# Optimization experiments

Measured on AMD Instinct MI355X. Metric: run time of the kernel, lower is better.

Reference implementation:

```python
import jax, jax.numpy as jnp
import numpy as np

B, T, C, NH = 8, 1024, 1024, 16
DH = C // NH  # 64


def setup_inputs() -> dict:
    key = jax.random.key(0)
    ks = jax.random.split(key, 7)
    s = 1.0 / np.sqrt(C)
    return {
        "x": jax.random.normal(ks[0], (B, T, C), dtype=jnp.float32),
        "Wq": jax.random.normal(ks[1], (C, C), dtype=jnp.float32) * s,
        "bq": jnp.zeros((C,), dtype=jnp.float32),
        "Wk": jax.random.normal(ks[2], (C, C), dtype=jnp.float32) * s,
        "bk": jnp.zeros((C,), dtype=jnp.float32),
        "Wv": jax.random.normal(ks[3], (C, C), dtype=jnp.float32) * s,
        "bv": jnp.zeros((C,), dtype=jnp.float32),
    }


def reference(x, Wq, bq, Wk, bk, Wv, bv):
    # Linear projections (weights stored as [in, out])
    q = x @ Wq + bq  # [B, T, C]
    k = x @ Wk + bk
    v = x @ Wv + bv
    q = q.reshape(B, T, NH, DH)
    k = k.reshape(B, T, NH, DH)
    v = v.reshape(B, T, NH, DH)
    scale = 1.0 / np.sqrt(DH)
    # NOTE: source module's causal mask buffer is all-ones due to a non-inplace
    # masked_fill bug, so attention is NON-causal (mask multiply is a no-op).
    attn = jnp.einsum("bqhd,bkhd->bhqk", q, k) * scale  # [B, NH, T, T]
    attn = jax.nn.softmax(attn, axis=-1)
    # dropout is identity (p=0 / eval)
    o = jnp.einsum("bhqk,bkhd->bqhd", attn, v)  # [B, T, NH, DH]
    return o.reshape(B, T, C)
```

## Files before the change

### kernel.cpp

```cpp
#include <hip/hip_runtime.h>


#define B_  8
#define T_  1024
#define C_  1024
#define NH_ 16
#define DH_ 64
#define M_  (B_ * T_)

typedef __bf16 bf16x8 __attribute__((ext_vector_type(8)));
typedef float  floatx4 __attribute__((ext_vector_type(4)));
typedef float  floatx16 __attribute__((ext_vector_type(16)));
typedef unsigned int uintx4 __attribute__((ext_vector_type(4)));

__device__ __forceinline__ unsigned short f2bf(float f) {
    unsigned int u = __float_as_uint(f);
    unsigned int r = (u + 0x7fffu + ((u >> 16) & 1u)) >> 16;
    return (unsigned short)r;
}

__device__ __forceinline__ unsigned int f2bf2(float a, float b) {
    unsigned int ua = __float_as_uint(a), ub = __float_as_uint(b);
    ua += 0x7fffu + ((ua >> 16) & 1u);
    ub += 0x7fffu + ((ub >> 16) & 1u);
#if __has_builtin(__builtin_amdgcn_perm)
    return __builtin_amdgcn_perm(ub, ua, 0x07060302u);
#else
    return (ua >> 16) | (ub & 0xffff0000u);
#endif
}

__device__ __forceinline__ void gload_lds16(const void* g, void* l) {
    __builtin_amdgcn_global_load_lds(
        (const __attribute__((address_space(1))) unsigned int*)g,
        (__attribute__((address_space(3))) unsigned int*)l, 16, 0, 0);
}

__global__ __launch_bounds__(256) void prep_kernel(
    const float* __restrict__ x, unsigned short* __restrict__ xb,
    const float* __restrict__ Wq, const float* __restrict__ Wk,
    const float* __restrict__ Wv, unsigned short* __restrict__ WtAll)
{
    int blk = blockIdx.x;
    if (blk < 8192) {
        int i = blk * 256 + threadIdx.x;
        float4 v = ((const float4*)x)[i];
        ushort4 o;
        unsigned int lo = f2bf2(v.x, v.y), hi = f2bf2(v.z, v.w);
        o.x = (unsigned short)lo; o.y = (unsigned short)(lo >> 16);
        o.z = (unsigned short)hi; o.w = (unsigned short)(hi >> 16);
        ((ushort4*)xb)[i] = o;
        return;
    }
    int tb3 = blk - 8192;
    int which = tb3 >> 8;
    int tb = tb3 & 255;
    const float* W = (which == 0) ? Wq : ((which == 1) ? Wk : Wv);
    unsigned short* out = WtAll + (size_t)which * C_ * C_;

    __shared__ __align__(16) unsigned short tile[64 * 68];
    int k0 = (tb >> 4) * 64, n0 = (tb & 15) * 64;
    int c = threadIdx.x & 63, r0 = threadIdx.x >> 6;

    for (int j = 0; j < 16; ++j) {
        int r = r0 + j * 4;
        tile[c * 68 + r] = f2bf(W[(size_t)(k0 + r) * C_ + n0 + c]);
    }
    __syncthreads();
    int k4 = (threadIdx.x & 15) * 4;
    int nw = threadIdx.x >> 4;
    for (int it = 0; it < 4; ++it) {
        int n = nw + it * 16;
        ushort4 o = *(const ushort4*)&tile[n * 68 + k4];
        *(ushort4*)&out[(size_t)(n0 + n) * C_ + k0 + k4] = o;
    }
}

__global__ __launch_bounds__(256) void qkv_gemm_kernel(
    const unsigned short* __restrict__ xb,
    const unsigned short* __restrict__ WtAll,
    const float* __restrict__ bq, const float* __restrict__ bk,
    const float* __restrict__ bv,
    unsigned short* __restrict__ Qb, unsigned short* __restrict__ Kb,
    unsigned short* __restrict__ Vt)
{
    int which = blockIdx.z;
    const unsigned short* W = WtAll + (size_t)which * C_ * C_;
    const float* bias = (which == 0) ? bq : ((which == 1) ? bk : bv);
    float oscale = (which == 0) ? 0.125f * 1.44269504f : 1.0f;

    __shared__ __align__(16) unsigned short As[128 * 64];
    __shared__ __align__(16) unsigned short Bs[128 * 64];

    int tid = threadIdx.x;
    int wave = tid >> 6, lane = tid & 63;
    int quad = lane >> 4, l16 = lane & 15, l7 = l16 & 7;
    int wm = wave >> 1, wn = wave & 1;
    int bm = blockIdx.x, bn = blockIdx.y;

    floatx4 acc[4][4] = {};

    for (int kk = 0; kk < C_; kk += 64) {
        __syncthreads();
        #pragma unroll
        for (int i = 0; i < 4; ++i) {
            int c = (wave * 4 + i) * 64 + lane;
            int row = c >> 3;
            int lcol = ((c & 7) ^ (row & 7)) * 8;
            gload_lds16(&xb[(size_t)(bm * 128 + row) * C_ + kk + lcol],
                        &As[(wave * 4 + i) * 512]);
            gload_lds16(&W[(size_t)(bn * 128 + row) * C_ + kk + lcol],
                        &Bs[(wave * 4 + i) * 512]);
        }
        __syncthreads();
        #pragma unroll
        for (int s = 0; s < 2; ++s) {
            bf16x8 a[4], bfr[4];
            #pragma unroll
            for (int mt = 0; mt < 4; ++mt) {
                int row = wm * 64 + mt * 16 + l16;
                a[mt] = *(const bf16x8*)&As[row * 64 + ((s * 4 + quad) ^ l7) * 8];
            }
            #pragma unroll
            for (int nt = 0; nt < 4; ++nt) {
                int row = wn * 64 + nt * 16 + l16;
                bfr[nt] = *(const bf16x8*)&Bs[row * 64 + ((s * 4 + quad) ^ l7) * 8];
            }
            if (which < 2) {
                #pragma unroll
                for (int mt = 0; mt < 4; ++mt)
                    #pragma unroll
                    for (int nt = 0; nt < 4; ++nt)
                        acc[mt][nt] = __builtin_amdgcn_mfma_f32_16x16x32_bf16(
                            bfr[nt], a[mt], acc[mt][nt], 0, 0, 0);
            } else {
                #pragma unroll
                for (int mt = 0; mt < 4; ++mt)
                    #pragma unroll
                    for (int nt = 0; nt < 4; ++nt)
                        acc[mt][nt] = __builtin_amdgcn_mfma_f32_16x16x32_bf16(
                            a[mt], bfr[nt], acc[mt][nt], 0, 0, 0);
            }
        }
    }

    if (which < 2) {
        unsigned short* outp = (which == 0) ? Qb : Kb;
        #pragma unroll
        for (int mt = 0; mt < 4; ++mt) {
            int tg = bm * 128 + wm * 64 + mt * 16 + l16;
            int bb = tg >> 10, t = tg & (T_ - 1);
            #pragma unroll
            for (int nt = 0; nt < 4; ++nt) {
                int colg = bn * 128 + wn * 64 + nt * 16 + quad * 4;
                int h = colg >> 6, d = colg & 63;
                float4 b4 = *(const float4*)&bias[colg];
                uint2 o;
                o.x = f2bf2((acc[mt][nt][0] + b4.x) * oscale,
                            (acc[mt][nt][1] + b4.y) * oscale);
                o.y = f2bf2((acc[mt][nt][2] + b4.z) * oscale,
                            (acc[mt][nt][3] + b4.w) * oscale);
                *(uint2*)&outp[((size_t)(bb * NH_ + h) * T_ + t) * DH_ + d] = o;
            }
        }
    } else {
        #pragma unroll
        for (int nt = 0; nt < 4; ++nt) {
            int colg = bn * 128 + wn * 64 + nt * 16 + l16;
            int h = colg >> 6, d = colg & 63;
            float bval = bias[colg];
            #pragma unroll
            for (int mt = 0; mt < 4; ++mt) {
                int tg = bm * 128 + wm * 64 + mt * 16 + quad * 4;
                int bb = tg >> 10, t = tg & (T_ - 1);
                uint2 o;
                o.x = f2bf2(acc[mt][nt][0] + bval, acc[mt][nt][1] + bval);
                o.y = f2bf2(acc[mt][nt][2] + bval, acc[mt][nt][3] + bval);
                *(uint2*)&Vt[((size_t)(bb * NH_ + h) * DH_ + d) * T_ + t] = o;
            }
        }
    }
}

__global__ __launch_bounds__(256) void attn_kernel(
    const unsigned short* __restrict__ Qb,
    const unsigned short* __restrict__ Kb,
    const unsigned short* __restrict__ Vt,
    float* __restrict__ out)
{
    int bh = blockIdx.x;
    int qblk = blockIdx.y;
    int b = bh >> 4, h = bh & (NH_ - 1);
    int tid = threadIdx.x;
    int wave = tid >> 6, lane = tid & 63;
    int l5 = lane & 31, hi = lane >> 5;

    const unsigned short* Qh = Qb + (size_t)bh * T_ * DH_;
    const unsigned short* Kh = Kb + (size_t)bh * T_ * DH_;
    const unsigned short* Vh = Vt + (size_t)bh * DH_ * T_;

    __shared__ __align__(16) unsigned short Ks[128 * 64];
    __shared__ __align__(16) unsigned short Vs[64 * 128];

    int qrow = qblk * 128 + wave * 32 + l5;
    bf16x8 qa[4];
    #pragma unroll
    for (int sl = 0; sl < 4; ++sl)
        qa[sl] = *(const bf16x8*)&Qh[(size_t)qrow * DH_ + sl * 16 + hi * 8];

    floatx16 o_acc[2] = {};
    float l_i = 0.0f;

    for (int kt2 = 0; kt2 < T_ / 128; ++kt2) {
        __syncthreads();
        #pragma unroll
        for (int i = 0; i < 4; ++i) {
            int c = (wave * 4 + i) * 64 + lane;
            int krow = c >> 3;
            int klcol = ((c & 7) ^ (krow & 7)) * 8;
            gload_lds16(&Kh[(size_t)(kt2 * 128 + krow) * DH_ + klcol],
                        &Ks[(wave * 4 + i) * 512]);
            int vrow = c >> 4;
            int vlcol = ((c & 15) ^ (vrow & 15)) * 8;
            gload_lds16(&Vh[(size_t)vrow * T_ + kt2 * 128 + vlcol],
                        &Vs[(wave * 4 + i) * 512]);
        }
        __syncthreads();

        #pragma unroll
        for (int kh = 0; kh < 2; ++kh) {
            #pragma unroll
            for (int nt = 0; nt < 2; ++nt) {
                floatx16 st = {};
                int r = kh * 64 + nt * 32 + l5;
                #pragma unroll
                for (int sl = 0; sl < 4; ++sl) {
                    bf16x8 kb = *(const bf16x8*)&Ks[r * 64 + ((sl * 2 + hi) ^ (r & 7)) * 8];
                    st = __builtin_amdgcn_mfma_f32_32x32x16_bf16(kb, qa[sl], st, 0, 0, 0);
                }

                unsigned int pd[8];
                float rs = 0.0f;
                #pragma unroll
                for (int m = 0; m < 8; ++m) {
                    float e0 = exp2f(st[2 * m]);
                    float e1 = exp2f(st[2 * m + 1]);
                    rs += e0 + e1;
                    pd[m] = f2bf2(e0, e1);
                }
                l_i += rs;

                #pragma unroll
                for (int ks2 = 0; ks2 < 2; ++ks2) {
                    int base = ks2 * 4;
                    uintx4 pbu;
                    {
                        unsigned int c0 = pd[base + 0], c2 = pd[base + 2];
                        unsigned int uk = hi ? c2 : c0;
                        unsigned int us = hi ? c0 : c2;
                        unsigned int rr = (unsigned int)__shfl_xor((int)us, 32);
                        pbu.x = hi ? rr : uk;
                        pbu.z = hi ? uk : rr;
                        unsigned int c1 = pd[base + 1], c3 = pd[base + 3];
                        uk = hi ? c3 : c1;
                        us = hi ? c1 : c3;
                        rr = (unsigned int)__shfl_xor((int)us, 32);
                        pbu.y = hi ? rr : uk;
                        pbu.w = hi ? uk : rr;
                    }
                    bf16x8 pb = __builtin_bit_cast(bf16x8, pbu);
                    int ch = (kh * 4 + nt * 2 + ks2) * 2 + hi;
                    #pragma unroll
                    for (int dt = 0; dt < 2; ++dt) {
                        int vr = dt * 32 + l5;
                        bf16x8 vb = *(const bf16x8*)&Vs[vr * 128 + (ch ^ (vr & 15)) * 8];
                        o_acc[dt] = __builtin_amdgcn_mfma_f32_32x32x16_bf16(
                            vb, pb, o_acc[dt], 0, 0, 0);
                    }
                }
            }
        }
    }

    float lt = l_i + __shfl_xor(l_i, 32);
    float inv = 1.0f / lt;
    int t = qblk * 128 + wave * 32 + l5;
    float* op = &out[((size_t)b * T_ + t) * C_ + h * DH_];
    #pragma unroll
    for (int dt = 0; dt < 2; ++dt) {
        #pragma unroll
        for (int g = 0; g < 4; ++g) {
            float4 v;
            v.x = o_acc[dt][g * 4 + 0] * inv;
            v.y = o_acc[dt][g * 4 + 1] * inv;
            v.z = o_acc[dt][g * 4 + 2] * inv;
            v.w = o_acc[dt][g * 4 + 3] * inv;
            *(float4*)&op[dt * 32 + g * 8 + hi * 4] = v;
        }
    }
}

extern "C" void kernel_launch(void* const* d_in, const int* in_sizes, int n_in,
                              void* d_out, int out_size, void* d_ws, size_t ws_size,
                              hipStream_t stream) {
    const float* x  = (const float*)d_in[0];
    const float* Wq = (const float*)d_in[1];
    const float* bq = (const float*)d_in[2];
    const float* Wk = (const float*)d_in[3];
    const float* bk = (const float*)d_in[4];
    const float* Wv = (const float*)d_in[5];
    const float* bv = (const float*)d_in[6];
    float* out = (float*)d_out;

    char* ws = (char*)d_ws;
    size_t off = 0;
    unsigned short* xb = (unsigned short*)(ws + off); off += (size_t)M_ * C_ * 2;
    unsigned short* Wt = (unsigned short*)(ws + off); off += (size_t)3 * C_ * C_ * 2;
    unsigned short* Qb = (unsigned short*)(ws + off); off += (size_t)M_ * C_ * 2;
    unsigned short* Kb = (unsigned short*)(ws + off); off += (size_t)M_ * C_ * 2;
    unsigned short* Vt = (unsigned short*)(ws + off); off += (size_t)M_ * C_ * 2;

    prep_kernel<<<dim3(8960), dim3(256), 0, stream>>>(x, xb, Wq, Wk, Wv, Wt);

    qkv_gemm_kernel<<<dim3(M_ / 128, C_ / 128, 3), dim3(256), 0, stream>>>(
        xb, Wt, bq, bk, bv, Qb, Kb, Vt);

    attn_kernel<<<dim3(B_ * NH_, T_ / 128), dim3(256), 0, stream>>>(Qb, Kb, Vt, out);
}
```

Baseline: 235.6 us.

## Double-buffer K/V tiles in attention and permute V layout to drop shuffles

Doubles the LDS buffers for K and V so the next tile's global-to-LDS loads are issued while the current tile is computed, leaving one barrier per iteration instead of two. It also permutes the token order when the projection kernel writes transposed V. That lets the P operand for the PV MFMA be built straight from registers, removing the cross-lane shuffles and selects. In exchange, LDS use doubles, which may lower occupancy, and correctness depends on the V permutation matching the MFMA output layout.

```diff
diff --git a/kernel.cpp b/kernel.cpp
--- a/kernel.cpp
+++ b/kernel.cpp
@@ -164,6 +164,7 @@
             }
         }
     } else {
+        int quadp = ((quad & 1) << 1) | (quad >> 1);
         #pragma unroll
         for (int nt = 0; nt < 4; ++nt) {
             int colg = bn * 128 + wn * 64 + nt * 16 + l16;
@@ -171,7 +172,7 @@
             float bval = bias[colg];
             #pragma unroll
             for (int mt = 0; mt < 4; ++mt) {
-                int tg = bm * 128 + wm * 64 + mt * 16 + quad * 4;
+                int tg = bm * 128 + wm * 64 + mt * 16 + quadp * 4;
                 int bb = tg >> 10, t = tg & (T_ - 1);
                 uint2 o;
                 o.x = f2bf2(acc[mt][nt][0] + bval, acc[mt][nt][1] + bval);
@@ -199,8 +200,8 @@
     const unsigned short* Kh = Kb + (size_t)bh * T_ * DH_;
     const unsigned short* Vh = Vt + (size_t)bh * DH_ * T_;
 
-    __shared__ __align__(16) unsigned short Ks[128 * 64];
-    __shared__ __align__(16) unsigned short Vs[64 * 128];
+    __shared__ __align__(16) unsigned short Ks[2][128 * 64];
+    __shared__ __align__(16) unsigned short Vs[2][64 * 128];
 
     int qrow = qblk * 128 + wave * 32 + l5;
     bf16x8 qa[4];
@@ -211,21 +212,26 @@
     floatx16 o_acc[2] = {};
     float l_i = 0.0f;
 
-    for (int kt2 = 0; kt2 < T_ / 128; ++kt2) {
-        __syncthreads();
+    auto stage = [&](int kt2, int bb) {
         #pragma unroll
         for (int i = 0; i < 4; ++i) {
             int c = (wave * 4 + i) * 64 + lane;
             int krow = c >> 3;
             int klcol = ((c & 7) ^ (krow & 7)) * 8;
             gload_lds16(&Kh[(size_t)(kt2 * 128 + krow) * DH_ + klcol],
-                        &Ks[(wave * 4 + i) * 512]);
+                        &Ks[bb][(wave * 4 + i) * 512]);
             int vrow = c >> 4;
             int vlcol = ((c & 15) ^ (vrow & 15)) * 8;
             gload_lds16(&Vh[(size_t)vrow * T_ + kt2 * 128 + vlcol],
-                        &Vs[(wave * 4 + i) * 512]);
-        }
+                        &Vs[bb][(wave * 4 + i) * 512]);
+        }
+    };
+
+    stage(0, 0);
+    for (int kt2 = 0; kt2 < T_ / 128; ++kt2) {
+        int cur = kt2 & 1;
         __syncthreads();
+        if (kt2 + 1 < T_ / 128) stage(kt2 + 1, cur ^ 1);
 
         #pragma unroll
         for (int kh = 0; kh < 2; ++kh) {
@@ -235,7 +241,7 @@
                 int r = kh * 64 + nt * 32 + l5;
                 #pragma unroll
                 for (int sl = 0; sl < 4; ++sl) {
-                    bf16x8 kb = *(const bf16x8*)&Ks[r * 64 + ((sl * 2 + hi) ^ (r & 7)) * 8];
+                    bf16x8 kb = *(const bf16x8*)&Ks[cur][r * 64 + ((sl * 2 + hi) ^ (r & 7)) * 8];
                     st = __builtin_amdgcn_mfma_f32_32x32x16_bf16(kb, qa[sl], st, 0, 0, 0);
                 }
 
@@ -252,28 +258,17 @@
 
                 #pragma unroll
                 for (int ks2 = 0; ks2 < 2; ++ks2) {
-                    int base = ks2 * 4;
                     uintx4 pbu;
-                    {
-                        unsigned int c0 = pd[base + 0], c2 = pd[base + 2];
-                        unsigned int uk = hi ? c2 : c0;
-                        unsigned int us = hi ? c0 : c2;
-                        unsigned int rr = (unsigned int)__shfl_xor((int)us, 32);
-                        pbu.x = hi ? rr : uk;
-                        pbu.z = hi ? uk : rr;
-                        unsigned int c1 = pd[base + 1], c3 = pd[base + 3];
-                        uk = hi ? c3 : c1;
-                        us = hi ? c1 : c3;
-                        rr = (unsigned int)__shfl_xor((int)us, 32);
-                        pbu.y = hi ? rr : uk;
-                        pbu.w = hi ? uk : rr;
-                    }
+                    pbu.x = pd[ks2 * 4 + 0];
+                    pbu.y = pd[ks2 * 4 + 1];
+                    pbu.z = pd[ks2 * 4 + 2];
+                    pbu.w = pd[ks2 * 4 + 3];
                     bf16x8 pb = __builtin_bit_cast(bf16x8, pbu);
-                    int ch = (kh * 4 + nt * 2 + ks2) * 2 + hi;
+                    int ch = kh * 8 + nt * 4 + ks2 * 2 + hi;
                     #pragma unroll
                     for (int dt = 0; dt < 2; ++dt) {
                         int vr = dt * 32 + l5;
-                        bf16x8 vb = *(const bf16x8*)&Vs[vr * 128 + (ch ^ (vr & 15)) * 8];
+                        bf16x8 vb = *(const bf16x8*)&Vs[cur][vr * 128 + (ch ^ (vr & 15)) * 8];
                         o_acc[dt] = __builtin_amdgcn_mfma_f32_32x32x16_bf16(
                             vb, pb, o_acc[dt], 0, 0, 0);
                     }
```

New measurement: 230.5 us. 1.02x faster.
